# Performance work log

Measured on AMD Instinct MI355X. Metric: run time of the kernel, lower is better.

The kernel has to match this reference:

```python
import jax, jax.numpy as jnp
import numpy as np

N_HEADS = 16
NEG_INF = -1e30  # stand-in for -inf, safe in fp32/bf16


def setup_inputs() -> dict:
    key = jax.random.key(0)
    k1, k2, k3, k4 = jax.random.split(key, 4)
    B, T, C = 8, 1024, 1024
    x = jax.random.normal(k1, (B, T, C), dtype=jnp.float32)
    # torch nn.Linear weight layout: [out_features, in_features]
    w_attn = jax.random.normal(k2, (3 * C, C), dtype=jnp.float32) * 0.02
    w_proj = jax.random.normal(k3, (C, C), dtype=jnp.float32) * 0.02
    b_proj = jax.random.normal(k4, (C,), dtype=jnp.float32) * 0.02
    return {"x": x, "w_attn": w_attn, "w_proj": w_proj, "b_proj": b_proj}


def reference(x, w_attn, w_proj, b_proj):
    B, T, C = x.shape
    H = N_HEADS
    d = C // H
    # fused QKV projection (bias=False); source splits as keys, queries, values
    qkv = x @ w_attn.T  # [B, T, 3C]
    k, q, v = jnp.split(qkv, 3, axis=-1)
    # [B, T, C] -> [B, H, T, d]
    k = k.reshape(B, T, H, d).transpose(0, 2, 1, 3)
    q = q.reshape(B, T, H, d).transpose(0, 2, 1, 3)
    v = v.reshape(B, T, H, d).transpose(0, 2, 1, 3)
    scale = 1.0 / jnp.sqrt(jnp.asarray(d, dtype=x.dtype))
    att = jnp.einsum('bhqd,bhkd->bhqk', q, k) * scale  # [B, H, T, T]
    causal = jnp.tril(jnp.ones((T, T), dtype=bool))
    att = jnp.where(causal, att, NEG_INF)
    att = jax.nn.softmax(att, axis=-1)
    y = jnp.einsum('bhqk,bhkd->bhqd', att, v)  # [B, H, T, d]
    y = y.transpose(0, 2, 1, 3).reshape(B, T, C)
    return y @ w_proj.T + b_proj
```

## Files before the change

### kernel.cpp

```cpp
#include <hip/hip_runtime.h>
#include <stdint.h>

typedef unsigned short u16;
typedef __attribute__((ext_vector_type(8))) short short8;
typedef __attribute__((ext_vector_type(4))) float f32x4;

__device__ __forceinline__ float bf2f(u16 u) {
    union { unsigned u; float f; } x; x.u = ((unsigned)u) << 16; return x.f;
}
__device__ __forceinline__ float bf_lo(unsigned w) {
    union { unsigned u; float f; } x; x.u = w << 16; return x.f;
}
__device__ __forceinline__ float bf_hi(unsigned w) {
    union { unsigned u; float f; } x; x.u = w & 0xffff0000u; return x.f;
}
__device__ __forceinline__ u16 f2bf(float f) {
    union { float f; unsigned u; } x; x.f = f;
    unsigned r = x.u + 0x7fffu + ((x.u >> 16) & 1u);
    return (u16)(r >> 16);
}
__device__ __forceinline__ uint4 cvt8(const float* p) {
    float4 a = *reinterpret_cast<const float4*>(p);
    float4 b = *reinterpret_cast<const float4*>(p + 4);
    uint4 r;
    r.x = (unsigned)f2bf(a.x) | ((unsigned)f2bf(a.y) << 16);
    r.y = (unsigned)f2bf(a.z) | ((unsigned)f2bf(a.w) << 16);
    r.z = (unsigned)f2bf(b.x) | ((unsigned)f2bf(b.y) << 16);
    r.w = (unsigned)f2bf(b.z) | ((unsigned)f2bf(b.w) << 16);
    return r;
}

__device__ __forceinline__ void gl16(const u16* g, u16* l) {
    __builtin_amdgcn_global_load_lds(
        (const __attribute__((address_space(1))) void*)g,
        (__attribute__((address_space(3))) void*)l, 16, 0, 0);
}

__global__ __launch_bounds__(256) void cvt_kernel(const float* __restrict__ in,
                                                  u16* __restrict__ out, int n8) {
    int i = blockIdx.x * 256 + threadIdx.x;
    if (i < n8) *reinterpret_cast<uint4*>(&out[(size_t)i * 8]) = cvt8(&in[(size_t)i * 8]);
}

__global__ __launch_bounds__(256) void cvt3_kernel(const float* __restrict__ a, int na8,
                                                   const float* __restrict__ b, int nb8,
                                                   const float* __restrict__ c, int nc8,
                                                   u16* __restrict__ dst) {
    int i = blockIdx.x * 256 + threadIdx.x;
    const float* src; int off;
    if (i < na8)            { src = a; off = i; }
    else if (i < na8 + nb8) { src = b; off = i - na8; }
    else if (i < na8 + nb8 + nc8) { src = c; off = i - na8 - nb8; }
    else return;
    *reinterpret_cast<uint4*>(&dst[(size_t)i * 8]) = cvt8(&src[(size_t)off * 8]);
}

#define BM 128
#define BN 128
#define BK 32
#define BKA 64

template<bool CF32>
__global__ __launch_bounds__(256) void gemm_bt_a(const u16* __restrict__ A,
                                                 const u16* __restrict__ W,
                                                 void* __restrict__ Cv,
                                                 const float* __restrict__ bias,
                                                 int M, int N, int K, int lda,
                                                 u16* __restrict__ vt) {
    __shared__ __align__(16) u16 As[BM * BKA];
    __shared__ __align__(16) u16 Ws[BN * BKA];

    const int tid  = threadIdx.x;
    const int lane = tid & 63;
    const int w    = tid >> 6;
    const int wr   = w >> 1;
    const int wc   = w & 1;
    const int quad = lane >> 4;
    const int l16  = lane & 15;

    const int row0 = blockIdx.y * BM;
    const int col0 = blockIdx.x * BN;

    const int srow = w * 8 + (lane >> 3);
    const int gc   = (lane & 7) ^ (lane >> 3);

    const u16* gA[4]; const u16* gW[4]; u16* lA[4]; u16* lW[4];
#pragma unroll
    for (int p = 0; p < 4; p++) {
        gA[p] = A + (size_t)(row0 + p * 32 + srow) * lda + gc * 8;
        gW[p] = W + (size_t)(col0 + p * 32 + srow) * K  + gc * 8;
        lA[p] = &As[(p * 32 + w * 8) * BKA];
        lW[p] = &Ws[(p * 32 + w * 8) * BKA];
    }

    const int cr0 = (quad ^ (l16 & 7)) * 8;

    f32x4 acc[4][4] = {};

    for (int k0 = 0; k0 < K; k0 += BKA) {
        __syncthreads();
#pragma unroll
        for (int p = 0; p < 4; p++) {
            gl16(gA[p] + k0, lA[p]);
            gl16(gW[p] + k0, lW[p]);
        }
        __syncthreads();

#pragma unroll
        for (int ks = 0; ks < 2; ks++) {
            const int cc = cr0 ^ (ks * 32);
            short8 af[4], bfr[4];
#pragma unroll
            for (int i = 0; i < 4; i++)
                af[i] = *reinterpret_cast<const short8*>(&As[(wr * 64 + i * 16 + l16) * BKA + cc]);
#pragma unroll
            for (int j = 0; j < 4; j++)
                bfr[j] = *reinterpret_cast<const short8*>(&Ws[(wc * 64 + j * 16 + l16) * BKA + cc]);
#pragma unroll
            for (int i = 0; i < 4; i++)
#pragma unroll
                for (int j = 0; j < 4; j++)
                    acc[i][j] = __builtin_amdgcn_mfma_f32_16x16x32_bf16(af[i], bfr[j], acc[i][j], 0, 0, 0);
        }
    }

    if (vt != nullptr && col0 >= 2048) {
        const int b = row0 >> 10;
#pragma unroll
        for (int j = 0; j < 4; j++) {
            const int hd = col0 - 2048 + wc * 64 + j * 16 + l16;
            u16* dstc = vt + (size_t)(b * 1024 + hd) * 1024 + (row0 & 1023) + wr * 64;
#pragma unroll
            for (int i = 0; i < 4; i++) {
                const int t0 = i * 16 + quad * 4;
                u16 pk[4];
#pragma unroll
                for (int r = 0; r < 4; r++) pk[r] = f2bf(acc[i][j][r]);
                *reinterpret_cast<uint2*>(dstc + t0) = *reinterpret_cast<uint2*>(pk);
            }
        }
    } else {
#pragma unroll
        for (int j = 0; j < 4; j++) {
            const int col = col0 + wc * 64 + j * 16 + l16;
            const float bval = bias ? bias[col] : 0.0f;
#pragma unroll
            for (int i = 0; i < 4; i++) {
#pragma unroll
                for (int r = 0; r < 4; r++) {
                    const int row = row0 + wr * 64 + i * 16 + quad * 4 + r;
                    if (CF32) ((float*)Cv)[(size_t)row * N + col] = acc[i][j][r] + bval;
                    else      ((u16*)Cv)[(size_t)row * N + col]  = f2bf(acc[i][j][r] + bval);
                }
            }
        }
    }
}

template<bool AF32, bool WF32, bool CF32>
__global__ __launch_bounds__(256) void gemm_bt(const void* __restrict__ Av,
                                               const void* __restrict__ Wv,
                                               void* __restrict__ Cv,
                                               const float* __restrict__ bias,
                                               int M, int N, int K, int lda) {
    __shared__ __align__(16) u16 As[BM * BK];
    __shared__ __align__(16) u16 Ws[BN * BK];

    const int tid  = threadIdx.x;
    const int lane = tid & 63;
    const int wave = tid >> 6;
    const int wr   = wave >> 1;
    const int wc   = wave & 1;
    const int quad = lane >> 4;
    const int l16  = lane & 15;

    const int row0 = blockIdx.y * BM;
    const int col0 = blockIdx.x * BN;

    const int sr = tid >> 2;
    const int sc = (tid & 3) * 8;

    f32x4 acc[4][4] = {};

    for (int k0 = 0; k0 < K; k0 += BK) {
        __syncthreads();
        if (AF32) {
            const float* A = (const float*)Av;
            *reinterpret_cast<uint4*>(&As[(sr)      * BK + sc]) = cvt8(&A[(size_t)(row0 + sr)      * lda + k0 + sc]);
            *reinterpret_cast<uint4*>(&As[(sr + 64) * BK + sc]) = cvt8(&A[(size_t)(row0 + sr + 64) * lda + k0 + sc]);
        } else {
            const u16* A = (const u16*)Av;
            *reinterpret_cast<uint4*>(&As[(sr)      * BK + sc]) =
                *reinterpret_cast<const uint4*>(&A[(size_t)(row0 + sr)      * lda + k0 + sc]);
            *reinterpret_cast<uint4*>(&As[(sr + 64) * BK + sc]) =
                *reinterpret_cast<const uint4*>(&A[(size_t)(row0 + sr + 64) * lda + k0 + sc]);
        }
        if (WF32) {
            const float* W = (const float*)Wv;
            *reinterpret_cast<uint4*>(&Ws[(sr)      * BK + sc]) = cvt8(&W[(size_t)(col0 + sr)      * K + k0 + sc]);
            *reinterpret_cast<uint4*>(&Ws[(sr + 64) * BK + sc]) = cvt8(&W[(size_t)(col0 + sr + 64) * K + k0 + sc]);
        } else {
            const u16* W = (const u16*)Wv;
            *reinterpret_cast<uint4*>(&Ws[(sr)      * BK + sc]) =
                *reinterpret_cast<const uint4*>(&W[(size_t)(col0 + sr)      * K + k0 + sc]);
            *reinterpret_cast<uint4*>(&Ws[(sr + 64) * BK + sc]) =
                *reinterpret_cast<const uint4*>(&W[(size_t)(col0 + sr + 64) * K + k0 + sc]);
        }
        __syncthreads();

        short8 af[4], bfr[4];
#pragma unroll
        for (int i = 0; i < 4; i++)
            af[i] = *reinterpret_cast<const short8*>(&As[(wr * 64 + i * 16 + l16) * BK + quad * 8]);
#pragma unroll
        for (int j = 0; j < 4; j++)
            bfr[j] = *reinterpret_cast<const short8*>(&Ws[(wc * 64 + j * 16 + l16) * BK + quad * 8]);

#pragma unroll
        for (int i = 0; i < 4; i++)
#pragma unroll
            for (int j = 0; j < 4; j++)
                acc[i][j] = __builtin_amdgcn_mfma_f32_16x16x32_bf16(af[i], bfr[j], acc[i][j], 0, 0, 0);
    }

#pragma unroll
    for (int j = 0; j < 4; j++) {
        const int col = col0 + wc * 64 + j * 16 + l16;
        const float bval = bias ? bias[col] : 0.0f;
#pragma unroll
        for (int i = 0; i < 4; i++) {
#pragma unroll
            for (int r = 0; r < 4; r++) {
                const int row = row0 + wr * 64 + i * 16 + quad * 4 + r;
                if (CF32) ((float*)Cv)[(size_t)row * N + col] = acc[i][j][r] + bval;
                else      ((u16*)Cv)[(size_t)row * N + col]  = f2bf(acc[i][j][r] + bval);
            }
        }
    }
}

__global__ __launch_bounds__(256) void vtrans_kernel(const u16* __restrict__ qkv,
                                                     u16* __restrict__ vt) {
    const int bid = blockIdx.x;
    const int tt = bid & 15, h = (bid >> 4) & 15, b = bid >> 8;
    const int t0 = tt * 64;
    __shared__ __align__(16) u16 tile[64 * 72];
    const int tr = threadIdx.x >> 2, tc = (threadIdx.x & 3) * 16;
    const u16* src = qkv + (size_t)(b * 1024 + t0 + tr) * 3072 + 2048 + h * 64 + tc;
    *reinterpret_cast<uint4*>(&tile[tr * 72 + tc])     = *reinterpret_cast<const uint4*>(src);
    *reinterpret_cast<uint4*>(&tile[tr * 72 + tc + 8]) = *reinterpret_cast<const uint4*>(src + 8);
    __syncthreads();
    const int dh = tr, t1 = tc;
    __align__(16) u16 buf[16];
#pragma unroll
    for (int i = 0; i < 16; i++) buf[i] = tile[(t1 + i) * 72 + dh];
    u16* dst = vt + ((size_t)(b * 16 + h) * 64 + dh) * 1024 + t0 + t1;
    *reinterpret_cast<uint4*>(dst)     = *reinterpret_cast<uint4*>(&buf[0]);
    *reinterpret_cast<uint4*>(dst + 8) = *reinterpret_cast<uint4*>(&buf[8]);
}

#define SK 72

__global__ __launch_bounds__(256) void fattn_kernel(u16* __restrict__ qkv,
                                                    const u16* __restrict__ vt) {
    __shared__ __align__(16) u16 Ks[64 * SK];
    __shared__ __align__(16) u16 Vs[64 * SK];
    __shared__ __align__(16) u16 Ps[4][32 * SK];
    __shared__ __align__(16) float aS[4][32];

    const int tid  = threadIdx.x;
    const int lane = tid & 63;
    const int w    = tid >> 6;
    const int quad = lane >> 4;
    const int l16  = lane & 15;

    const int bid = blockIdx.x;
    const int qt  = 7 - (bid >> 7);
    const int bh  = bid & 127;
    const int b   = bh >> 4;
    const int h   = bh & 15;

    u16* qb        = qkv + (size_t)b * 1024 * 3072;
    const u16* vtb = vt + (size_t)bh * 64 * 1024;

    const int qrow0 = qt * 128 + w * 32;

    short8 qf[2][2];
#pragma unroll
    for (int mj = 0; mj < 2; mj++)
#pragma unroll
        for (int ks = 0; ks < 2; ks++) {
            const u16* src = qb + (size_t)(qrow0 + mj * 16 + l16) * 3072 + 1024 + h * 64 + ks * 32 + quad * 8;
            __align__(16) u16 tmp[8];
            *reinterpret_cast<uint4*>(tmp) = *reinterpret_cast<const uint4*>(src);
#pragma unroll
            for (int e = 0; e < 8; e++) tmp[e] = f2bf(bf2f(tmp[e]) * 0.125f);
            qf[mj][ks] = *reinterpret_cast<short8*>(tmp);
        }

    f32x4 oa[2][4] = {};
    float m_run[2] = {-1e30f, -1e30f};
    float l_run[2] = {0.f, 0.f};

    const int jtmax = 2 * qt + 1;
    for (int jt = 0; jt <= jtmax; jt++) {
        const int j0 = jt * 64;
        __syncthreads();
        {
            const int sr = tid >> 2, sc = (tid & 3) * 8;
            const u16* kg = qb + (size_t)(j0 + sr) * 3072 + h * 64;
            *reinterpret_cast<uint4*>(&Ks[sr * SK + sc])      = *reinterpret_cast<const uint4*>(kg + sc);
            *reinterpret_cast<uint4*>(&Ks[sr * SK + sc + 32]) = *reinterpret_cast<const uint4*>(kg + sc + 32);
            const u16* vg = vtb + (size_t)sr * 1024 + j0;
            *reinterpret_cast<uint4*>(&Vs[sr * SK + sc])      = *reinterpret_cast<const uint4*>(vg + sc);
            *reinterpret_cast<uint4*>(&Vs[sr * SK + sc + 32]) = *reinterpret_cast<const uint4*>(vg + sc + 32);
        }
        __syncthreads();

        if (j0 > qrow0 + 31) continue;

        f32x4 s[4][2] = {};
#pragma unroll
        for (int ks = 0; ks < 2; ks++) {
            short8 kf[4];
#pragma unroll
            for (int ti = 0; ti < 4; ti++)
                kf[ti] = *reinterpret_cast<const short8*>(&Ks[(ti * 16 + l16) * SK + ks * 32 + quad * 8]);
#pragma unroll
            for (int ti = 0; ti < 4; ti++)
#pragma unroll
                for (int mj = 0; mj < 2; mj++)
                    s[ti][mj] = __builtin_amdgcn_mfma_f32_16x16x32_bf16(kf[ti], qf[mj][ks], s[ti][mj], 0, 0, 0);
        }

        const bool need_mask = (j0 + 63 > qrow0);
#pragma unroll
        for (int mj = 0; mj < 2; mj++) {
            const int mg = qrow0 + mj * 16 + l16;
            if (need_mask) {
#pragma unroll
                for (int ti = 0; ti < 4; ti++)
#pragma unroll
                    for (int r = 0; r < 4; r++)
                        if (j0 + ti * 16 + quad * 4 + r > mg) s[ti][mj][r] = -1e30f;
            }
            float mt = -1e30f;
#pragma unroll
            for (int ti = 0; ti < 4; ti++)
#pragma unroll
                for (int r = 0; r < 4; r++) mt = fmaxf(mt, s[ti][mj][r]);
            mt = fmaxf(mt, __shfl_xor(mt, 16));
            mt = fmaxf(mt, __shfl_xor(mt, 32));
            const float mn    = fmaxf(m_run[mj], mt);
            const float alpha = __expf(m_run[mj] - mn);
            m_run[mj] = mn;
            float ls = 0.f;
#pragma unroll
            for (int ti = 0; ti < 4; ti++)
#pragma unroll
                for (int r = 0; r < 4; r++) {
                    const float p = __expf(s[ti][mj][r] - mn);
                    s[ti][mj][r] = p;
                    ls += p;
                }
            ls += __shfl_xor(ls, 16);
            ls += __shfl_xor(ls, 32);
            l_run[mj] = l_run[mj] * alpha + ls;
            if (lane < 16) aS[w][mj * 16 + l16] = alpha;
#pragma unroll
            for (int ti = 0; ti < 4; ti++) {
                uint2 pk;
                pk.x = (unsigned)f2bf(s[ti][mj][0]) | ((unsigned)f2bf(s[ti][mj][1]) << 16);
                pk.y = (unsigned)f2bf(s[ti][mj][2]) | ((unsigned)f2bf(s[ti][mj][3]) << 16);
                *reinterpret_cast<uint2*>(&Ps[w][(mj * 16 + l16) * SK + ti * 16 + quad * 4]) = pk;
            }
        }

#pragma unroll
        for (int mi = 0; mi < 2; mi++) {
            const f32x4 av = *reinterpret_cast<const f32x4*>(&aS[w][mi * 16 + quad * 4]);
#pragma unroll
            for (int nd = 0; nd < 4; nd++)
#pragma unroll
                for (int r = 0; r < 4; r++) oa[mi][nd][r] *= av[r];
        }

#pragma unroll
        for (int ks = 0; ks < 2; ks++) {
            short8 pf[2], vf[4];
#pragma unroll
            for (int mi = 0; mi < 2; mi++)
                pf[mi] = *reinterpret_cast<const short8*>(&Ps[w][(mi * 16 + l16) * SK + ks * 32 + quad * 8]);
#pragma unroll
            for (int nd = 0; nd < 4; nd++)
                vf[nd] = *reinterpret_cast<const short8*>(&Vs[(nd * 16 + l16) * SK + ks * 32 + quad * 8]);
#pragma unroll
            for (int mi = 0; mi < 2; mi++)
#pragma unroll
                for (int nd = 0; nd < 4; nd++)
                    oa[mi][nd] = __builtin_amdgcn_mfma_f32_16x16x32_bf16(pf[mi], vf[nd], oa[mi][nd], 0, 0, 0);
        }
    }

    if (lane < 16) { aS[w][l16] = 1.f / l_run[0]; aS[w][16 + l16] = 1.f / l_run[1]; }
#pragma unroll
    for (int mi = 0; mi < 2; mi++) {
        const f32x4 iv = *reinterpret_cast<const f32x4*>(&aS[w][mi * 16 + quad * 4]);
#pragma unroll
        for (int nd = 0; nd < 4; nd++)
#pragma unroll
            for (int r = 0; r < 4; r++) {
                const int row = qrow0 + mi * 16 + quad * 4 + r;
                qb[(size_t)row * 3072 + 1024 + h * 64 + nd * 16 + l16] = f2bf(oa[mi][nd][r] * iv[r]);
            }
    }
}

__global__ __launch_bounds__(256) void attn_kernel(u16* __restrict__ qkv) {
    const int g  = blockIdx.x * 256 + threadIdx.x;
    const int q  = g & 1023;
    const int bh = g >> 10;
    const int b  = bh >> 4;
    const int h  = bh & 15;
    const size_t base = (size_t)b * 1024 * 3072 + (size_t)h * 64;
    float qv[64];
    {
        const uint4* q4 = reinterpret_cast<const uint4*>(qkv + base + (size_t)q * 3072 + 1024);
#pragma unroll
        for (int c = 0; c < 8; c++) {
            uint4 t = q4[c];
            qv[c*8+0]=bf_lo(t.x); qv[c*8+1]=bf_hi(t.x); qv[c*8+2]=bf_lo(t.y); qv[c*8+3]=bf_hi(t.y);
            qv[c*8+4]=bf_lo(t.z); qv[c*8+5]=bf_hi(t.z); qv[c*8+6]=bf_lo(t.w); qv[c*8+7]=bf_hi(t.w);
        }
    }
    float o[64];
#pragma unroll
    for (int i = 0; i < 64; i++) o[i] = 0.0f;
    float m = -1e30f, l = 0.0f;
    const int jmax = q | 63;
    for (int j = 0; j <= jmax; j++) {
        const uint4* k4 = reinterpret_cast<const uint4*>(qkv + base + (size_t)j * 3072);
        float s = 0.0f;
#pragma unroll
        for (int c = 0; c < 8; c++) {
            uint4 t = k4[c];
            s += qv[c*8+0]*bf_lo(t.x)+qv[c*8+1]*bf_hi(t.x)+qv[c*8+2]*bf_lo(t.y)+qv[c*8+3]*bf_hi(t.y)
               + qv[c*8+4]*bf_lo(t.z)+qv[c*8+5]*bf_hi(t.z)+qv[c*8+6]*bf_lo(t.w)+qv[c*8+7]*bf_hi(t.w);
        }
        s *= 0.125f;
        const bool act = (j <= q);
        if (!act) s = -1e30f;
        const float mn = fmaxf(m, s);
        const float alpha = __expf(m - mn);
        float p = __expf(s - mn);
        if (!act) p = 0.0f;
        l = l * alpha + p;
        const uint4* v4 = reinterpret_cast<const uint4*>(qkv + base + (size_t)j * 3072 + 2048);
#pragma unroll
        for (int c = 0; c < 8; c++) {
            uint4 t = v4[c];
            o[c*8+0]=o[c*8+0]*alpha+p*bf_lo(t.x); o[c*8+1]=o[c*8+1]*alpha+p*bf_hi(t.x);
            o[c*8+2]=o[c*8+2]*alpha+p*bf_lo(t.y); o[c*8+3]=o[c*8+3]*alpha+p*bf_hi(t.y);
            o[c*8+4]=o[c*8+4]*alpha+p*bf_lo(t.z); o[c*8+5]=o[c*8+5]*alpha+p*bf_hi(t.z);
            o[c*8+6]=o[c*8+6]*alpha+p*bf_lo(t.w); o[c*8+7]=o[c*8+7]*alpha+p*bf_hi(t.w);
        }
        m = mn;
    }
    const float inv = 1.0f / l;
    u16* yrow = qkv + base + (size_t)q * 3072 + 1024;
#pragma unroll
    for (int i = 0; i < 64; i++) yrow[i] = f2bf(o[i] * inv);
}

extern "C" void kernel_launch(void* const* d_in, const int* in_sizes, int n_in,
                              void* d_out, int out_size, void* d_ws, size_t ws_size,
                              hipStream_t stream) {
    const float* x      = (const float*)d_in[0];
    const float* w_attn = (const float*)d_in[1];
    const float* w_proj = (const float*)d_in[2];
    const float* b_proj = (const float*)d_in[3];
    float* out = (float*)d_out;

    const int M = 8192, K = 1024;
    const size_t QKV = (size_t)8192 * 3072;
    const size_t VT  = (size_t)8 * 16 * 64 * 1024;

    u16* qkv = (u16*)d_ws;
    u16* vtb = qkv + QKV;
    u16* xb  = vtb + VT;
    u16* wab = xb + (size_t)8192 * 1024;
    u16* wpb = wab + (size_t)3072 * 1024;

    const size_t need_full = (QKV + VT + (size_t)8192*1024 + (size_t)3072*1024 + (size_t)1024*1024) * 2;
    const size_t need_mid  = (QKV + VT) * 2;

    if (ws_size >= need_full) {
        cvt3_kernel<<<6144, 256, 0, stream>>>(x, 8192 * 1024 / 8,
                                              w_attn, 3072 * 1024 / 8,
                                              w_proj, 1024 * 1024 / 8, xb);
        gemm_bt_a<false><<<dim3(24, 64), 256, 0, stream>>>(xb, wab, qkv, nullptr, M, 3072, K, K, vtb);
        fattn_kernel<<<1024, 256, 0, stream>>>(qkv, vtb);
        gemm_bt_a<true><<<dim3(8, 64), 256, 0, stream>>>(qkv + 1024, wpb, out, b_proj, M, 1024, K, 3072, nullptr);
    } else if (ws_size >= need_mid) {
        gemm_bt<true, true, false><<<dim3(24, 64), 256, 0, stream>>>(x, w_attn, qkv, nullptr, M, 3072, K, K);
        vtrans_kernel<<<2048, 256, 0, stream>>>(qkv, vtb);
        fattn_kernel<<<1024, 256, 0, stream>>>(qkv, vtb);
        gemm_bt<false, true, true><<<dim3(8, 64), 256, 0, stream>>>(qkv + 1024, w_proj, out, b_proj, M, 1024, K, 3072);
    } else {
        gemm_bt<true, true, false><<<dim3(24, 64), 256, 0, stream>>>(x, w_attn, qkv, nullptr, M, 3072, K, K);
        attn_kernel<<<512, 256, 0, stream>>>(qkv);
        gemm_bt<false, true, true><<<dim3(8, 64), 256, 0, stream>>>(qkv + 1024, w_proj, out, b_proj, M, 1024, K, 3072);
    }
}
```

Before: 240.0 us.

## Add 8-wave triple-buffered 256x128 GEMM kernel for QKV and output projections

Introduces a new GEMM kernel with 512 threads, 256x128 tiles, and triple-buffered LDS loads that direct-load from global memory. Each k-step is split into two MFMA phases interleaved with the next tile's loads, using barriers and s_setprio. Both projection GEMMs use it in place of the 128x128 kernel. The intent is to raise MFMA utilisation by hiding global loads, at the cost of a large LDS footprint (144 KB across three stages) that limits occupancy. Halving the grid also risks poor tail balance on the smaller output projection.

After: 237.8 us. No clear change (-0.9%).

```diff
diff --git a/kernel.cpp b/kernel.cpp
--- a/kernel.cpp
+++ b/kernel.cpp
@@ -59,6 +59,154 @@
 #define BN 128
 #define BK 32
 #define BKA 64
+
+#define PBM 256
+#define PBN 128
+#define PBK 64
+
+template<bool CF32>
+__global__ __launch_bounds__(512, 2) void gemm8p(const u16* __restrict__ A,
+                                                 const u16* __restrict__ W,
+                                                 void* __restrict__ Cv,
+                                                 const float* __restrict__ bias,
+                                                 int M, int N, int K, int lda,
+                                                 u16* __restrict__ vt) {
+    __shared__ __align__(16) u16 As[3][PBM * PBK];
+    __shared__ __align__(16) u16 Ws[3][PBN * PBK];
+
+    const int tid  = threadIdx.x;
+    const int lane = tid & 63;
+    const int w    = tid >> 6;
+    const int wm   = w >> 1;
+    const int wn   = w & 1;
+    const int quad = lane >> 4;
+    const int l16  = lane & 15;
+
+    const int row0 = blockIdx.y * PBM;
+    const int col0 = blockIdx.x * PBN;
+
+    const int srow = w * 8 + (lane >> 3);
+    const int gc   = (lane & 7) ^ (lane >> 3);
+
+    const u16* gA[4]; const u16* gW[2];
+#pragma unroll
+    for (int p = 0; p < 4; p++) gA[p] = A + (size_t)(row0 + p * 64 + srow) * lda + gc * 8;
+#pragma unroll
+    for (int p = 0; p < 2; p++) gW[p] = W + (size_t)(col0 + p * 64 + srow) * K + gc * 8;
+
+    const int ldsoff = (w * 8) * PBK;
+
+    const int ro = l16 & 7;
+
+    f32x4 acc[4][4] = {};
+
+    const int NT = K / PBK;
+
+#pragma unroll
+    for (int p = 0; p < 4; p++) gl16(gA[p], &As[0][(p * 64) * PBK + ldsoff]);
+#pragma unroll
+    for (int p = 0; p < 2; p++) gl16(gW[p], &Ws[0][(p * 64) * PBK + ldsoff]);
+#pragma unroll
+    for (int p = 0; p < 4; p++) gl16(gA[p] + PBK, &As[1][(p * 64) * PBK + ldsoff]);
+#pragma unroll
+    for (int p = 0; p < 2; p++) gl16(gW[p] + PBK, &Ws[1][(p * 64) * PBK + ldsoff]);
+
+    int cb = 0, sb = 2;
+    for (int t = 0; t < NT; t++) {
+        const int kst = (t + 2 < NT ? t + 2 : NT - 1) * PBK;
+
+        asm volatile("s_waitcnt vmcnt(6)" ::: "memory");
+        __builtin_amdgcn_s_barrier();
+
+        short8 bfr[4][2], af0[2][2];
+#pragma unroll
+        for (int jj = 0; jj < 4; jj++)
+#pragma unroll
+            for (int ks = 0; ks < 2; ks++)
+                bfr[jj][ks] = *reinterpret_cast<const short8*>(
+                    &Ws[cb][(wn * 64 + jj * 16 + l16) * PBK + (((ks * 4 + quad) ^ ro) * 8)]);
+#pragma unroll
+        for (int ii = 0; ii < 2; ii++)
+#pragma unroll
+            for (int ks = 0; ks < 2; ks++)
+                af0[ii][ks] = *reinterpret_cast<const short8*>(
+                    &As[cb][(wm * 64 + ii * 16 + l16) * PBK + (((ks * 4 + quad) ^ ro) * 8)]);
+        gl16(gA[0] + kst, &As[sb][(0 * 64) * PBK + ldsoff]);
+        gl16(gA[1] + kst, &As[sb][(1 * 64) * PBK + ldsoff]);
+        gl16(gA[2] + kst, &As[sb][(2 * 64) * PBK + ldsoff]);
+        __builtin_amdgcn_s_barrier();
+        asm volatile("s_waitcnt lgkmcnt(0)" ::: "memory");
+        __builtin_amdgcn_s_setprio(1);
+#pragma unroll
+        for (int ks = 0; ks < 2; ks++)
+#pragma unroll
+            for (int ii = 0; ii < 2; ii++)
+#pragma unroll
+                for (int jj = 0; jj < 4; jj++)
+                    acc[ii][jj] = __builtin_amdgcn_mfma_f32_16x16x32_bf16(af0[ii][ks], bfr[jj][ks], acc[ii][jj], 0, 0, 0);
+        __builtin_amdgcn_s_setprio(0);
+        __builtin_amdgcn_s_barrier();
+
+        short8 af1[2][2];
+#pragma unroll
+        for (int ii = 0; ii < 2; ii++)
+#pragma unroll
+            for (int ks = 0; ks < 2; ks++)
+                af1[ii][ks] = *reinterpret_cast<const short8*>(
+                    &As[cb][(wm * 64 + (ii + 2) * 16 + l16) * PBK + (((ks * 4 + quad) ^ ro) * 8)]);
+        gl16(gA[3] + kst, &As[sb][(3 * 64) * PBK + ldsoff]);
+        gl16(gW[0] + kst, &Ws[sb][(0 * 64) * PBK + ldsoff]);
+        gl16(gW[1] + kst, &Ws[sb][(1 * 64) * PBK + ldsoff]);
+        __builtin_amdgcn_s_barrier();
+        asm volatile("s_waitcnt lgkmcnt(0)" ::: "memory");
+        __builtin_amdgcn_s_setprio(1);
+#pragma unroll
+        for (int ks = 0; ks < 2; ks++)
+#pragma unroll
+            for (int ii = 0; ii < 2; ii++)
+#pragma unroll
+                for (int jj = 0; jj < 4; jj++)
+                    acc[ii + 2][jj] = __builtin_amdgcn_mfma_f32_16x16x32_bf16(af1[ii][ks], bfr[jj][ks], acc[ii + 2][jj], 0, 0, 0);
+        __builtin_amdgcn_s_setprio(0);
+        __builtin_amdgcn_s_barrier();
+
+        cb = (cb + 1 == 3) ? 0 : cb + 1;
+        sb = (sb + 1 == 3) ? 0 : sb + 1;
+    }
+    asm volatile("s_waitcnt vmcnt(0)" ::: "memory");
+
+    if (vt != nullptr && col0 >= 2048) {
+        const int b = row0 >> 10;
+#pragma unroll
+        for (int jj = 0; jj < 4; jj++) {
+            const int hd = col0 - 2048 + wn * 64 + jj * 16 + l16;
+            u16* dstc = vt + (size_t)(b * 1024 + hd) * 1024 + (row0 & 1023) + wm * 64;
+#pragma unroll
+            for (int ii = 0; ii < 4; ii++) {
+                const int t0 = ii * 16 + quad * 4;
+                u16 pk[4];
+#pragma unroll
+                for (int r = 0; r < 4; r++) pk[r] = f2bf(acc[ii][jj][r]);
+                *reinterpret_cast<uint2*>(dstc + t0) = *reinterpret_cast<uint2*>(pk);
+            }
+        }
+    } else {
+#pragma unroll
+        for (int jj = 0; jj < 4; jj++) {
+            const int col = col0 + wn * 64 + jj * 16 + l16;
+            const float bval = bias ? bias[col] : 0.0f;
+#pragma unroll
+            for (int ii = 0; ii < 4; ii++) {
+#pragma unroll
+                for (int r = 0; r < 4; r++) {
+                    const int row = row0 + wm * 64 + ii * 16 + quad * 4 + r;
+                    if (CF32) ((float*)Cv)[(size_t)row * N + col] = acc[ii][jj][r] + bval;
+                    else      ((u16*)Cv)[(size_t)row * N + col]  = f2bf(acc[ii][jj][r] + bval);
+                }
+            }
+        }
+    }
+}
 
 template<bool CF32>
 __global__ __launch_bounds__(256) void gemm_bt_a(const u16* __restrict__ A,
@@ -498,9 +646,9 @@
         cvt3_kernel<<<6144, 256, 0, stream>>>(x, 8192 * 1024 / 8,
                                               w_attn, 3072 * 1024 / 8,
                                               w_proj, 1024 * 1024 / 8, xb);
-        gemm_bt_a<false><<<dim3(24, 64), 256, 0, stream>>>(xb, wab, qkv, nullptr, M, 3072, K, K, vtb);
+        gemm8p<false><<<dim3(24, 32), 512, 0, stream>>>(xb, wab, qkv, nullptr, M, 3072, K, K, vtb);
         fattn_kernel<<<1024, 256, 0, stream>>>(qkv, vtb);
-        gemm_bt_a<true><<<dim3(8, 64), 256, 0, stream>>>(qkv + 1024, wpb, out, b_proj, M, 1024, K, 3072, nullptr);
+        gemm8p<true><<<dim3(8, 32), 512, 0, stream>>>(qkv + 1024, wpb, out, b_proj, M, 1024, K, 3072, nullptr);
     } else if (ws_size >= need_mid) {
         gemm_bt<true, true, false><<<dim3(24, 64), 256, 0, stream>>>(x, w_attn, qkv, nullptr, M, 3072, K, K);
         vtrans_kernel<<<2048, 256, 0, stream>>>(qkv, vtb);
```

## Add 256x256-tile double-buffered GEMM kernel for the QKV projection

Applied to the files above, without the earlier changes.

Adds a new 512-thread GEMM kernel with 256x256 output tiles and a 64-wide K step. It double-buffers A and W tiles in LDS, using async global-to-LDS loads interleaved with four MFMA phases per K step, plus s_setprio and explicit waitcnt and barrier scheduling. The QKV projection now uses this kernel instead of the 128x128 one. The aim is more data reuse per tile and better overlap of memory loads with matrix math. The trade-off is 128KB of LDS per block, which limits occupancy, and a 384-block grid that may leave a partial wave.

New measurement: 261.6 us. 9.0% more time.

```diff
diff --git a/kernel.cpp b/kernel.cpp
--- a/kernel.cpp
+++ b/kernel.cpp
@@ -59,6 +59,146 @@
 #define BN 128
 #define BK 32
 #define BKA 64
+
+#define PBK 64
+
+template<bool CF32>
+__global__ __launch_bounds__(512, 2) void gemm256(const u16* __restrict__ A,
+                                                  const u16* __restrict__ W,
+                                                  void* __restrict__ Cv,
+                                                  const float* __restrict__ bias,
+                                                  int M, int N, int K, int lda,
+                                                  u16* __restrict__ vt) {
+    __shared__ __align__(16) u16 As[2][256 * PBK];
+    __shared__ __align__(16) u16 Ws[2][256 * PBK];
+
+    const int tid  = threadIdx.x;
+    const int lane = tid & 63;
+    const int w    = tid >> 6;
+    const int wm   = w >> 2;
+    const int wn   = w & 3;
+    const int quad = lane >> 4;
+    const int l16  = lane & 15;
+    const int ro   = l16 & 7;
+
+    const int row0 = blockIdx.y * 256;
+    const int col0 = blockIdx.x * 256;
+
+    const int srow = w * 8 + (lane >> 3);
+    const int gc   = (lane & 7) ^ (lane >> 3);
+    const int lub  = (w * 8) * PBK;
+
+    const u16* gA[4]; const u16* gW[4];
+#pragma unroll
+    for (int q = 0; q < 4; q++) {
+        gA[q] = A + (size_t)(row0 + q * 64 + srow) * lda + gc * 8;
+        gW[q] = W + (size_t)(col0 + q * 64 + srow) * K  + gc * 8;
+    }
+
+    f32x4 acc[8][4] = {};
+
+    const int NT = K / PBK;
+
+#pragma unroll
+    for (int q = 0; q < 4; q++) gl16(gA[q], &As[0][q * 64 * PBK + lub]);
+#pragma unroll
+    for (int q = 0; q < 4; q++) gl16(gW[q], &Ws[0][q * 64 * PBK + lub]);
+#pragma unroll
+    for (int q = 0; q < 4; q++) gl16(gW[q] + PBK, &Ws[1][q * 64 * PBK + lub]);
+    gl16(gA[0] + PBK, &As[1][0 * 64 * PBK + lub]);
+    gl16(gA[2] + PBK, &As[1][2 * 64 * PBK + lub]);
+    asm volatile("s_waitcnt vmcnt(6)" ::: "memory");
+    __builtin_amdgcn_s_barrier();
+
+#define READ_A(P)                                                              \
+    _Pragma("unroll") for (int im = 0; im < 2; im++)                           \
+    _Pragma("unroll") for (int ks = 0; ks < 2; ks++)                           \
+        af[im][ks] = *reinterpret_cast<const short8*>(                         \
+            &As[cb][(wm * 128 + (P) * 32 + im * 16 + l16) * PBK +              \
+                    (((ks * 4 + quad) ^ ro) * 8)]);
+
+#define PHASE_TAIL(IB)                                                         \
+    __builtin_amdgcn_s_barrier();                                              \
+    asm volatile("s_waitcnt lgkmcnt(0)" ::: "memory");                         \
+    __builtin_amdgcn_s_setprio(1);                                             \
+    _Pragma("unroll") for (int ks = 0; ks < 2; ks++)                           \
+    _Pragma("unroll") for (int im = 0; im < 2; im++)                           \
+    _Pragma("unroll") for (int jn = 0; jn < 4; jn++)                           \
+        acc[(IB) + im][jn] = __builtin_amdgcn_mfma_f32_16x16x32_bf16(          \
+            af[im][ks], bf[jn][ks], acc[(IB) + im][jn], 0, 0, 0);              \
+    __builtin_amdgcn_s_setprio(0);                                             \
+    __builtin_amdgcn_s_barrier();
+
+    for (int t = 0; t < NT; t++) {
+        const int cb = t & 1;
+        const int kA = (t + 1 < NT ? t + 1 : NT - 1) * PBK;
+        const int k2 = (t + 2 < NT ? t + 2 : NT - 1) * PBK;
+
+        short8 bf[4][2], af[2][2];
+
+#pragma unroll
+        for (int jn = 0; jn < 4; jn++)
+#pragma unroll
+            for (int ks = 0; ks < 2; ks++)
+                bf[jn][ks] = *reinterpret_cast<const short8*>(
+                    &Ws[cb][(wn * 64 + jn * 16 + l16) * PBK + (((ks * 4 + quad) ^ ro) * 8)]);
+        READ_A(0)
+        gl16(gA[1] + kA, &As[cb ^ 1][1 * 64 * PBK + lub]);
+        gl16(gA[3] + kA, &As[cb ^ 1][3 * 64 * PBK + lub]);
+        PHASE_TAIL(0)
+
+        READ_A(1)
+        gl16(gW[0] + k2, &Ws[cb][0 * 64 * PBK + lub]);
+        gl16(gW[1] + k2, &Ws[cb][1 * 64 * PBK + lub]);
+        PHASE_TAIL(2)
+
+        READ_A(2)
+        gl16(gW[2] + k2, &Ws[cb][2 * 64 * PBK + lub]);
+        gl16(gW[3] + k2, &Ws[cb][3 * 64 * PBK + lub]);
+        PHASE_TAIL(4)
+
+        READ_A(3)
+        gl16(gA[0] + k2, &As[cb][0 * 64 * PBK + lub]);
+        gl16(gA[2] + k2, &As[cb][2 * 64 * PBK + lub]);
+        asm volatile("s_waitcnt vmcnt(6)" ::: "memory");
+        PHASE_TAIL(6)
+    }
+#undef READ_A
+#undef PHASE_TAIL
+    asm volatile("s_waitcnt vmcnt(0)" ::: "memory");
+
+    if (vt != nullptr && col0 >= 2048) {
+        const int b = row0 >> 10;
+#pragma unroll
+        for (int jn = 0; jn < 4; jn++) {
+            const int hd = col0 - 2048 + wn * 64 + jn * 16 + l16;
+            u16* dstc = vt + (size_t)(b * 1024 + hd) * 1024 + (row0 & 1023) + wm * 128;
+#pragma unroll
+            for (int i = 0; i < 8; i++) {
+                const int t0 = i * 16 + quad * 4;
+                u16 pk[4];
+#pragma unroll
+                for (int r = 0; r < 4; r++) pk[r] = f2bf(acc[i][jn][r]);
+                *reinterpret_cast<uint2*>(dstc + t0) = *reinterpret_cast<uint2*>(pk);
+            }
+        }
+    } else {
+#pragma unroll
+        for (int jn = 0; jn < 4; jn++) {
+            const int col = col0 + wn * 64 + jn * 16 + l16;
+            const float bval = bias ? bias[col] : 0.0f;
+#pragma unroll
+            for (int i = 0; i < 8; i++) {
+#pragma unroll
+                for (int r = 0; r < 4; r++) {
+                    const int row = row0 + wm * 128 + i * 16 + quad * 4 + r;
+                    if (CF32) ((float*)Cv)[(size_t)row * N + col] = acc[i][jn][r] + bval;
+                    else      ((u16*)Cv)[(size_t)row * N + col]  = f2bf(acc[i][jn][r] + bval);
+                }
+            }
+        }
+    }
+}
 
 template<bool CF32>
 __global__ __launch_bounds__(256) void gemm_bt_a(const u16* __restrict__ A,
@@ -498,7 +638,7 @@
         cvt3_kernel<<<6144, 256, 0, stream>>>(x, 8192 * 1024 / 8,
                                               w_attn, 3072 * 1024 / 8,
                                               w_proj, 1024 * 1024 / 8, xb);
-        gemm_bt_a<false><<<dim3(24, 64), 256, 0, stream>>>(xb, wab, qkv, nullptr, M, 3072, K, K, vtb);
+        gemm256<false><<<dim3(12, 32), 512, 0, stream>>>(xb, wab, qkv, nullptr, M, 3072, K, K, vtb);
         fattn_kernel<<<1024, 256, 0, stream>>>(qkv, vtb);
         gemm_bt_a<true><<<dim3(8, 64), 256, 0, stream>>>(qkv + 1024, wpb, out, b_proj, M, 1024, K, 3072, nullptr);
     } else if (ws_size >= need_mid) {
```
